# Performance work log

Hardware: AMD Instinct MI355X
Metric: run time of the kernel (lower is better)

The kernel has to match this reference:

```python
import jax, jax.numpy as jnp
import numpy as np

N_NODES = 50000
HIDDEN = 512
N_EDGES = 200000
NUM_LAYERS = 2


def setup_inputs() -> dict:
    key = jax.random.key(0)
    ks = jax.random.split(key, 8)
    stdv = 1.0 / np.sqrt(HIDDEN)
    u = lambda k, shape: jax.random.uniform(k, shape, jnp.float32, -stdv, stdv)
    inputs = jnp.arange(N_NODES, dtype=jnp.int64)
    A = jax.random.randint(ks[0], (2, N_EDGES), 0, N_NODES, dtype=jnp.int64)
    emb = u(ks[1], (N_NODES, HIDDEN))            # embedding table
    weight = u(ks[2], (NUM_LAYERS, HIDDEN, HIDDEN))  # per-layer edge transform
    w_ih = u(ks[3], (3 * HIDDEN, HIDDEN))        # GRUCell input weights (r,z,n)
    w_hh = u(ks[4], (3 * HIDDEN, HIDDEN))        # GRUCell hidden weights
    b_ih = u(ks[5], (3 * HIDDEN,))
    b_hh = u(ks[6], (3 * HIDDEN,))
    return {"inputs": inputs, "A": A, "emb": emb, "weight": weight,
            "w_ih": w_ih, "w_hh": w_hh, "b_ih": b_ih, "b_hh": b_hh}


def _gru_cell(m, h, w_ih, w_hh, b_ih, b_hh):
    # torch.nn.GRUCell math, gate order (r, z, n)
    gi = m @ w_ih.T + b_ih
    gh = h @ w_hh.T + b_hh
    i_r, i_z, i_n = jnp.split(gi, 3, axis=-1)
    h_r, h_z, h_n = jnp.split(gh, 3, axis=-1)
    r = jax.nn.sigmoid(i_r + h_r)
    z = jax.nn.sigmoid(i_z + h_z)
    n = jnp.tanh(i_n + r * h_n)
    return (1.0 - z) * n + z * h


def reference(inputs, A, emb, weight, w_ih, w_hh, b_ih, b_hh):
    x = emb[inputs]                      # [N, C] embedding gather
    src, dst = A[0], A[1]
    n = x.shape[0]
    for l in range(NUM_LAYERS):
        m = x @ weight[l]                # [N, C] per-layer transform
        agg = jax.ops.segment_sum(m[src], dst, num_segments=n)  # scatter-add messages
        x = _gru_cell(agg, x, w_ih, w_hh, b_ih, b_hh)
    return x
```

## Files before the change

### kernel.cpp

```cpp
#include <hip/hip_runtime.h>
#include <stdint.h>

#define N_NODES 50000
#define HIDDEN  512
#define N_EDGES 200000

#define BK 32
#define LDP 40
#define NBX ((N_NODES + 127) / 128)

typedef __attribute__((ext_vector_type(8)))  short short8;
typedef __attribute__((ext_vector_type(4)))  float floatx4;
typedef __attribute__((ext_vector_type(16))) float floatx16;

__device__ inline float bf2f(ushort u) {
    union { uint32_t u; float f; } v; v.u = ((uint32_t)u) << 16; return v.f;
}
__device__ inline ushort f2bf(float f) {
    union { float f; uint32_t u; } v; v.f = f;
    uint32_t r = v.u + 0x7fffu + ((v.u >> 16) & 1u);
    return (ushort)(r >> 16);
}
__device__ inline floatx4 mfma16(short8 a, short8 b, floatx4 c) {
    return __builtin_amdgcn_mfma_f32_16x16x32_bf16(a, b, c, 0, 0, 0);
}
__device__ inline floatx16 mfma32(short8 a, short8 b, floatx16 c) {
    return __builtin_amdgcn_mfma_f32_32x32x16_bf16(a, b, c, 0, 0, 0);
}
__device__ inline void gld16(const void* g, void* l) {
    __builtin_amdgcn_global_load_lds(
        (const __attribute__((address_space(1))) unsigned int*)g,
        (__attribute__((address_space(3))) unsigned int*)l, 16, 0, 0);
}
__device__ inline bool idx_is64(const int* __restrict__ inputs) {
    return inputs[1] == 0 && inputs[2] == 1;
}

__global__ void k_gather(const int* __restrict__ inputs, const float* __restrict__ emb,
                         ushort* __restrict__ xb) {
    bool is64 = idx_is64(inputs);
    int t = blockIdx.x * blockDim.x + threadIdx.x;
    int row = t >> 6, s8 = (t & 63) << 3;
    if (row >= N_NODES) return;
    int srow = is64 ? inputs[2 * row] : inputs[row];
    srow = srow < 0 ? 0 : (srow >= N_NODES ? N_NODES - 1 : srow);
    const float* src = emb + (size_t)srow * HIDDEN + s8;
    float4 v0 = *(const float4*)(src);
    float4 v1 = *(const float4*)(src + 4);
    ushort o[8] = { f2bf(v0.x), f2bf(v0.y), f2bf(v0.z), f2bf(v0.w),
                    f2bf(v1.x), f2bf(v1.y), f2bf(v1.z), f2bf(v1.w) };
    *(uint4*)(xb + (size_t)row * HIDDEN + s8) = *(uint4*)o;
}

__global__ void k_cvt8(const float* __restrict__ src, ushort* __restrict__ dst, int n) {
    int t = blockIdx.x * blockDim.x + threadIdx.x;
    int base = t * 8;
    if (base >= n) return;
    float4 v0 = *(const float4*)(src + base);
    float4 v1 = *(const float4*)(src + base + 4);
    ushort o[8] = { f2bf(v0.x), f2bf(v0.y), f2bf(v0.z), f2bf(v0.w),
                    f2bf(v1.x), f2bf(v1.y), f2bf(v1.z), f2bf(v1.w) };
    *(uint4*)(dst + base) = *(uint4*)o;
}

__device__ inline size_t wf_index(int grow, int k) {
    int g3 = grow >> 9, gcol = grow & 511;
    int cb = gcol >> 5, llo = gcol & 31;
    int kk = k >> 4, hi = (k >> 3) & 1, jj = k & 7;
    return ((((size_t)g3 * 16 + cb) * 32 + kk) * 64 + llo + hi * 32) * 8 + jj;
}

__global__ __launch_bounds__(256) void k_gemm_w(const ushort* __restrict__ Aw,
                                                const ushort* __restrict__ Bw,
                                                ushort* __restrict__ Cw) {
    __shared__ ushort As[128][LDP];
    __shared__ ushort Bs[128][LDP];
    const int l = blockIdx.z;
    const ushort* Bp = Bw + (size_t)l * HIDDEN * HIDDEN;
    ushort* Cp = Cw + (size_t)l * 3 * HIDDEN * HIDDEN;
    const int n0 = blockIdx.x * 128, c0 = blockIdx.y * 128;
    const int t = threadIdx.x;
    const int wave = t >> 6, lane = t & 63;
    const int wm = (wave >> 1) << 6, wn = (wave & 1) << 6;
    const int fr = lane & 15, fk = (lane >> 4) << 3;
    const int lm = t >> 2, lk = (t & 3) << 3;
    floatx4 acc[4][4] = {};

    for (int k0 = 0; k0 < HIDDEN; k0 += BK) {
        *(uint4*)&As[lm][lk]      = *(const uint4*)(Aw + (size_t)(n0 + lm) * HIDDEN + k0 + lk);
        *(uint4*)&As[64 + lm][lk] = *(const uint4*)(Aw + (size_t)(n0 + 64 + lm) * HIDDEN + k0 + lk);
        *(uint4*)&Bs[lm][lk]      = *(const uint4*)(Bp + (size_t)(c0 + lm) * HIDDEN + k0 + lk);
        *(uint4*)&Bs[64 + lm][lk] = *(const uint4*)(Bp + (size_t)(c0 + 64 + lm) * HIDDEN + k0 + lk);
        __syncthreads();
        short8 aa[4], bb[4];
        #pragma unroll
        for (int i = 0; i < 4; ++i) {
            aa[i] = *(const short8*)&As[wm + i * 16 + fr][fk];
            bb[i] = *(const short8*)&Bs[wn + i * 16 + fr][fk];
        }
        #pragma unroll
        for (int i = 0; i < 4; ++i)
            #pragma unroll
            for (int j = 0; j < 4; ++j)
                acc[i][j] = mfma16(aa[i], bb[j], acc[i][j]);
        __syncthreads();
    }
    const int er = (lane >> 4) << 2, ec = lane & 15;
    #pragma unroll
    for (int i = 0; i < 4; ++i)
        #pragma unroll
        for (int j = 0; j < 4; ++j)
            #pragma unroll
            for (int r = 0; r < 4; ++r) {
                int grow = n0 + wm + i * 16 + er + r;
                int kcol = c0 + wn + j * 16 + ec;
                Cp[wf_index(grow, kcol)] = f2bf(acc[i][j][r]);
            }
}

__global__ void k_pack_hh(const float* __restrict__ whh, ushort* __restrict__ wfh) {
    int t = blockIdx.x * blockDim.x + threadIdx.x;
    if (t >= 3 * HIDDEN * HIDDEN / 8) return;
    int grow = t >> 6, k = (t & 63) << 3;
    const float* src = whh + (size_t)grow * HIDDEN + k;
    ushort o[8];
    #pragma unroll
    for (int j = 0; j < 8; ++j) o[j] = f2bf(src[j]);
    *(uint4*)(wfh + wf_index(grow, k)) = *(uint4*)o;
}

__global__ void k_hist(const int* __restrict__ inputs, const int* __restrict__ A,
                       int* __restrict__ count) {
    bool is64 = idx_is64(inputs);
    int e = blockIdx.x * blockDim.x + threadIdx.x;
    if (e >= N_EDGES) return;
    int d = is64 ? A[2 * (N_EDGES + e)] : A[N_EDGES + e];
    if (d < 0 || d >= N_NODES) return;
    atomicAdd(count + d, 1);
}

#define SCAN_T 1024
__global__ __launch_bounds__(SCAN_T) void k_scan(const int* __restrict__ count,
                                                 int* __restrict__ row_start,
                                                 int* __restrict__ cursor) {
    __shared__ int part[SCAN_T];
    const int t = threadIdx.x;
    const int chunk = (N_NODES + SCAN_T - 1) / SCAN_T;
    const int base = t * chunk;
    int s = 0;
    for (int i = 0; i < chunk; ++i) {
        int idx = base + i;
        if (idx < N_NODES) s += count[idx];
    }
    part[t] = s;
    __syncthreads();
    for (int off = 1; off < SCAN_T; off <<= 1) {
        int add = (t >= off) ? part[t - off] : 0;
        __syncthreads();
        part[t] += add;
        __syncthreads();
    }
    int running = (t == 0) ? 0 : part[t - 1];
    for (int i = 0; i < chunk; ++i) {
        int idx = base + i;
        if (idx < N_NODES) {
            row_start[idx] = running;
            cursor[idx] = running;
            running += count[idx];
        }
    }
    if (t == 0) row_start[N_NODES] = part[SCAN_T - 1];
}

__global__ void k_place(const int* __restrict__ inputs, const int* __restrict__ A,
                        int* __restrict__ cursor, int* __restrict__ esrc) {
    bool is64 = idx_is64(inputs);
    int e = blockIdx.x * blockDim.x + threadIdx.x;
    if (e >= N_EDGES) return;
    int s, d;
    if (is64) { s = A[2 * e]; d = A[2 * (N_EDGES + e)]; }
    else      { s = A[e];     d = A[N_EDGES + e]; }
    if (s < 0 || s >= N_NODES || d < 0 || d >= N_NODES) return;
    int pos = atomicAdd(cursor + d, 1);
    esrc[pos] = s;
}

__global__ __launch_bounds__(256) void k_agg(const int* __restrict__ row_start,
                                             const int* __restrict__ esrc,
                                             const ushort* __restrict__ x,
                                             ushort* __restrict__ ax) {
    int node = blockIdx.x * 4 + (threadIdx.x >> 6);
    if (node >= N_NODES) return;
    int lane = threadIdx.x & 63;
    int q = lane << 3;
    int beg = row_start[node], end = row_start[node + 1];
    float acc[8] = {};
    for (int i = beg; i < end; ++i) {
        int s = esrc[i];
        uint4 v = *(const uint4*)(x + (size_t)s * HIDDEN + q);
        const ushort* u = (const ushort*)&v;
        #pragma unroll
        for (int j = 0; j < 8; ++j) acc[j] += bf2f(u[j]);
    }
    ushort o[8];
    #pragma unroll
    for (int j = 0; j < 8; ++j) o[j] = f2bf(acc[j]);
    *(uint4*)(ax + (size_t)node * HIDDEN + q) = *(uint4*)o;
}

template<bool F32OUT>
__global__ __launch_bounds__(256, 2) void k_gru5(
    const ushort* __restrict__ agg, const ushort* __restrict__ xb_cur,
    const ushort* __restrict__ wfc,
    const ushort* __restrict__ wfh,
    const float* __restrict__ b_ih, const float* __restrict__ b_hh,
    ushort* __restrict__ outB, float* __restrict__ outF)
{
    __shared__ ushort S[2 * 20480];
    const int x  = blockIdx.x & 7;
    const int n  = blockIdx.x >> 3;
    const int by = n & 7;
    const int bx = x + ((n >> 3) << 3);
    if (bx >= NBX) return;
    const int n0 = bx * 128;
    const int t = threadIdx.x, w = t >> 6, lane = t & 63;
    const int lrow = lane & 31, lhi = lane >> 5;
    const int wr = w >> 1, wc = w & 1;
    const int wrow = wr << 6;
    const int cb = by * 2 + wc;

    floatx16 a_sr[2] = {}, a_sz[2] = {}, a_in[2] = {}, a_hn[2] = {};

    const ushort* wB[6] = { wfc, wfc + 262144, wfc + 524288,
                            wfh, wfh + 262144, wfh + 524288 };

    const ushort* sp[10];
    int           adv[10];
    int           off[10];
    #pragma unroll
    for (int q = 0; q < 10; ++q) {
        const int F = w * 10 + q;
        const int kk = F / 20, s = F % 20;
        off[q] = kk * 10240 + s * 512;
        if (s < 8) {
            const int rg = s & 3;
            int row = n0 + rg * 32 + lrow;
            if (row >= N_NODES) row = N_NODES - 1;
            const ushort* arr = (s < 4) ? agg : xb_cur;
            sp[q] = arr + (size_t)row * HIDDEN + kk * 16 + lhi * 8;
            adv[q] = 32;
        } else {
            const int g = (s - 8) >> 1, c = (s - 8) & 1;
            const int cbq = by * 2 + c;
            sp[q] = wB[g] + ((size_t)(cbq * 32 + kk) * 64 + lane) * 8;
            adv[q] = 1024;
        }
    }

    #pragma unroll
    for (int q = 0; q < 10; ++q) { gld16(sp[q], S + off[q]); sp[q] += adv[q]; }
    __syncthreads();

    for (int ks = 0; ks < 16; ++ks) {
        const int cur = ks & 1;
        if (ks + 1 < 16) {
            ushort* dst = S + (cur ^ 1) * 20480;
            #pragma unroll
            for (int q = 0; q < 10; ++q) { gld16(sp[q], dst + off[q]); sp[q] += adv[q]; }
        }
        const ushort* Bb = S + cur * 20480 + (size_t)lane * 8;
        #pragma unroll
        for (int kk = 0; kk < 2; ++kk) {
            const ushort* P = Bb + kk * 10240;
            short8 av0 = *(const short8*)(P + (wr * 2 + 0) * 512);
            short8 av1 = *(const short8*)(P + (wr * 2 + 1) * 512);
            short8 xv0 = *(const short8*)(P + (4 + wr * 2 + 0) * 512);
            short8 xv1 = *(const short8*)(P + (4 + wr * 2 + 1) * 512);
            short8 B0 = *(const short8*)(P + (8 +  0 + wc) * 512);
            short8 B1 = *(const short8*)(P + (8 +  2 + wc) * 512);
            short8 B2 = *(const short8*)(P + (8 +  4 + wc) * 512);
            short8 B3 = *(const short8*)(P + (8 +  6 + wc) * 512);
            short8 B4 = *(const short8*)(P + (8 +  8 + wc) * 512);
            short8 B5 = *(const short8*)(P + (8 + 10 + wc) * 512);
            a_sr[0] = mfma32(av0, B0, a_sr[0]);  a_sr[0] = mfma32(xv0, B3, a_sr[0]);
            a_sr[1] = mfma32(av1, B0, a_sr[1]);  a_sr[1] = mfma32(xv1, B3, a_sr[1]);
            a_sz[0] = mfma32(av0, B1, a_sz[0]);  a_sz[0] = mfma32(xv0, B4, a_sz[0]);
            a_sz[1] = mfma32(av1, B1, a_sz[1]);  a_sz[1] = mfma32(xv1, B4, a_sz[1]);
            a_in[0] = mfma32(av0, B2, a_in[0]);  a_in[1] = mfma32(av1, B2, a_in[1]);
            a_hn[0] = mfma32(xv0, B5, a_hn[0]);  a_hn[1] = mfma32(xv1, B5, a_hn[1]);
        }
        __syncthreads();
    }
    const int colL = (cb << 5) + lrow;
    const float bir = b_ih[colL] + b_hh[colL];
    const float biz = b_ih[HIDDEN + colL] + b_hh[HIDDEN + colL];
    const float bin = b_ih[2 * HIDDEN + colL];
    const float bhn = b_hh[2 * HIDDEN + colL];
    #pragma unroll
    for (int rf = 0; rf < 2; ++rf) {
        #pragma unroll
        for (int rg = 0; rg < 16; ++rg) {
            const int row = n0 + wrow + rf * 32 + (rg & 3) + ((rg >> 2) << 3) + (lhi << 2);
            if (row >= N_NODES) continue;
            float vsr = a_sr[rf][rg] + bir;
            float vsz = a_sz[rf][rg] + biz;
            float vin = a_in[rf][rg] + bin;
            float vhn = a_hn[rf][rg] + bhn;
            float rr = 1.f / (1.f + __expf(-vsr));
            float zz = 1.f / (1.f + __expf(-vsz));
            float nn = tanhf(vin + rr * vhn);
            float h  = bf2f(xb_cur[(size_t)row * HIDDEN + colL]);
            float out = (1.f - zz) * nn + zz * h;
            if (F32OUT) outF[(size_t)row * HIDDEN + colL] = out;
            else        outB[(size_t)row * HIDDEN + colL] = f2bf(out);
        }
    }
}

extern "C" void kernel_launch(void* const* d_in, const int* in_sizes, int n_in,
                              void* d_out, int out_size, void* d_ws, size_t ws_size,
                              hipStream_t stream) {
    const int*   inputs = (const int*)d_in[0];
    const int*   A      = (const int*)d_in[1];
    const float* emb    = (const float*)d_in[2];
    const float* weight = (const float*)d_in[3];
    const float* w_ih   = (const float*)d_in[4];
    const float* w_hh   = (const float*)d_in[5];
    const float* b_ih   = (const float*)d_in[6];
    const float* b_hh   = (const float*)d_in[7];

    char* ws = (char*)d_ws;
    size_t off = 0;
    auto alloc = [&](size_t bytes) { void* p = ws + off; off += (bytes + 255) & ~255ull; return p; };
    ushort* WihB      = (ushort*)alloc((size_t)3 * HIDDEN * HIDDEN * sizeof(ushort));
    ushort* Wb        = (ushort*)alloc((size_t)2 * HIDDEN * HIDDEN * sizeof(ushort));
    ushort* WFc       = (ushort*)alloc((size_t)2 * 3 * HIDDEN * HIDDEN * sizeof(ushort));
    ushort* WFhh      = (ushort*)alloc((size_t)3 * HIDDEN * HIDDEN * sizeof(ushort));
    ushort* bufA      = (ushort*)alloc((size_t)N_NODES * HIDDEN * sizeof(ushort));
    ushort* bufB      = (ushort*)alloc((size_t)N_NODES * HIDDEN * sizeof(ushort));
    int*    count     = (int*)alloc((size_t)N_NODES * sizeof(int));
    int*    row_start = (int*)alloc((size_t)(N_NODES + 1) * sizeof(int));
    int*    cursor    = (int*)alloc((size_t)N_NODES * sizeof(int));
    int*    esrc      = (int*)alloc((size_t)N_EDGES * sizeof(int));
    ushort* ax0       = (ushort*)d_out;

    const int nW3 = 3 * HIDDEN * HIDDEN, nW2 = 2 * HIDDEN * HIDDEN;
    const size_t WF_L = (size_t)3 * HIDDEN * HIDDEN;

    k_cvt8<<<(nW3 / 8 + 255) / 256, 256, 0, stream>>>(w_ih, WihB, nW3);
    k_cvt8<<<(nW2 / 8 + 255) / 256, 256, 0, stream>>>(weight, Wb, nW2);
    k_pack_hh<<<(nW3 / 8 + 255) / 256, 256, 0, stream>>>(w_hh, WFhh);
    k_gemm_w<<<dim3(12, 4, 2), 256, 0, stream>>>(WihB, Wb, WFc);

    k_gather<<<(N_NODES * 64 + 255) / 256, 256, 0, stream>>>(inputs, emb, bufA);

    hipMemsetAsync(count, 0, (size_t)N_NODES * sizeof(int), stream);
    k_hist<<<(N_EDGES + 255) / 256, 256, 0, stream>>>(inputs, A, count);
    k_scan<<<1, SCAN_T, 0, stream>>>(count, row_start, cursor);
    k_place<<<(N_EDGES + 255) / 256, 256, 0, stream>>>(inputs, A, cursor, esrc);

    dim3 gGru(8 * 8 * ((NBX + 7) / 8));
    dim3 ga((N_NODES + 3) / 4);

    k_agg<<<ga, 256, 0, stream>>>(row_start, esrc, bufA, ax0);
    k_gru5<false><<<gGru, 256, 0, stream>>>(ax0, bufA, WFc, WFhh, b_ih, b_hh, bufB, nullptr);

    k_agg<<<ga, 256, 0, stream>>>(row_start, esrc, bufB, bufA);
    k_gru5<true><<<gGru, 256, 0, stream>>>(bufA, bufB, WFc + WF_L, WFhh, b_ih, b_hh,
                                           nullptr, (float*)d_out);
}
```

Baseline: 932.5 us.

## Load GRU GEMM operands directly from global memory instead of LDS staging

The fused GRU GEMM kernel stops staging activation and weight fragments through a double-buffered LDS tile with global_load_lds and barriers. Each wave now loads its MFMA operands straight from global memory into registers in a 32-step unrolled loop. This removes the LDS traffic and block-wide synchronisation. In exchange, tiles shared between waves are no longer reused through LDS, which increases global and L2 load traffic and leaves latency hiding to the unrolled loads.

```diff
diff --git a/kernel.cpp b/kernel.cpp
--- a/kernel.cpp
+++ b/kernel.cpp
@@ -26,11 +26,6 @@
 }
 __device__ inline floatx16 mfma32(short8 a, short8 b, floatx16 c) {
     return __builtin_amdgcn_mfma_f32_32x32x16_bf16(a, b, c, 0, 0, 0);
-}
-__device__ inline void gld16(const void* g, void* l) {
-    __builtin_amdgcn_global_load_lds(
-        (const __attribute__((address_space(1))) unsigned int*)g,
-        (__attribute__((address_space(3))) unsigned int*)l, 16, 0, 0);
 }
 __device__ inline bool idx_is64(const int* __restrict__ inputs) {
     return inputs[1] == 0 && inputs[2] == 1;
@@ -209,14 +204,13 @@
 }
 
 template<bool F32OUT>
-__global__ __launch_bounds__(256, 2) void k_gru5(
+__global__ __launch_bounds__(256, 2) void k_gru7(
     const ushort* __restrict__ agg, const ushort* __restrict__ xb_cur,
     const ushort* __restrict__ wfc,
     const ushort* __restrict__ wfh,
     const float* __restrict__ b_ih, const float* __restrict__ b_hh,
     ushort* __restrict__ outB, float* __restrict__ outF)
 {
-    __shared__ ushort S[2 * 20480];
     const int x  = blockIdx.x & 7;
     const int n  = blockIdx.x >> 3;
     const int by = n & 7;
@@ -231,66 +225,40 @@
 
     floatx16 a_sr[2] = {}, a_sz[2] = {}, a_in[2] = {}, a_hn[2] = {};
 
-    const ushort* wB[6] = { wfc, wfc + 262144, wfc + 524288,
-                            wfh, wfh + 262144, wfh + 524288 };
-
-    const ushort* sp[10];
-    int           adv[10];
-    int           off[10];
-    #pragma unroll
-    for (int q = 0; q < 10; ++q) {
-        const int F = w * 10 + q;
-        const int kk = F / 20, s = F % 20;
-        off[q] = kk * 10240 + s * 512;
-        if (s < 8) {
-            const int rg = s & 3;
-            int row = n0 + rg * 32 + lrow;
-            if (row >= N_NODES) row = N_NODES - 1;
-            const ushort* arr = (s < 4) ? agg : xb_cur;
-            sp[q] = arr + (size_t)row * HIDDEN + kk * 16 + lhi * 8;
-            adv[q] = 32;
-        } else {
-            const int g = (s - 8) >> 1, c = (s - 8) & 1;
-            const int cbq = by * 2 + c;
-            sp[q] = wB[g] + ((size_t)(cbq * 32 + kk) * 64 + lane) * 8;
-            adv[q] = 1024;
-        }
-    }
-
-    #pragma unroll
-    for (int q = 0; q < 10; ++q) { gld16(sp[q], S + off[q]); sp[q] += adv[q]; }
-    __syncthreads();
-
-    for (int ks = 0; ks < 16; ++ks) {
-        const int cur = ks & 1;
-        if (ks + 1 < 16) {
-            ushort* dst = S + (cur ^ 1) * 20480;
-            #pragma unroll
-            for (int q = 0; q < 10; ++q) { gld16(sp[q], dst + off[q]); sp[q] += adv[q]; }
-        }
-        const ushort* Bb = S + cur * 20480 + (size_t)lane * 8;
-        #pragma unroll
-        for (int kk = 0; kk < 2; ++kk) {
-            const ushort* P = Bb + kk * 10240;
-            short8 av0 = *(const short8*)(P + (wr * 2 + 0) * 512);
-            short8 av1 = *(const short8*)(P + (wr * 2 + 1) * 512);
-            short8 xv0 = *(const short8*)(P + (4 + wr * 2 + 0) * 512);
-            short8 xv1 = *(const short8*)(P + (4 + wr * 2 + 1) * 512);
-            short8 B0 = *(const short8*)(P + (8 +  0 + wc) * 512);
-            short8 B1 = *(const short8*)(P + (8 +  2 + wc) * 512);
-            short8 B2 = *(const short8*)(P + (8 +  4 + wc) * 512);
-            short8 B3 = *(const short8*)(P + (8 +  6 + wc) * 512);
-            short8 B4 = *(const short8*)(P + (8 +  8 + wc) * 512);
-            short8 B5 = *(const short8*)(P + (8 + 10 + wc) * 512);
-            a_sr[0] = mfma32(av0, B0, a_sr[0]);  a_sr[0] = mfma32(xv0, B3, a_sr[0]);
-            a_sr[1] = mfma32(av1, B0, a_sr[1]);  a_sr[1] = mfma32(xv1, B3, a_sr[1]);
-            a_sz[0] = mfma32(av0, B1, a_sz[0]);  a_sz[0] = mfma32(xv0, B4, a_sz[0]);
-            a_sz[1] = mfma32(av1, B1, a_sz[1]);  a_sz[1] = mfma32(xv1, B4, a_sz[1]);
-            a_in[0] = mfma32(av0, B2, a_in[0]);  a_in[1] = mfma32(av1, B2, a_in[1]);
-            a_hn[0] = mfma32(xv0, B5, a_hn[0]);  a_hn[1] = mfma32(xv1, B5, a_hn[1]);
-        }
-        __syncthreads();
-    }
+    int r0 = n0 + wrow + lrow;       if (r0 >= N_NODES) r0 = N_NODES - 1;
+    int r1 = n0 + wrow + 32 + lrow;  if (r1 >= N_NODES) r1 = N_NODES - 1;
+    const ushort* pa0 = agg    + (size_t)r0 * HIDDEN + lhi * 8;
+    const ushort* pa1 = agg    + (size_t)r1 * HIDDEN + lhi * 8;
+    const ushort* px0 = xb_cur + (size_t)r0 * HIDDEN + lhi * 8;
+    const ushort* px1 = xb_cur + (size_t)r1 * HIDDEN + lhi * 8;
+    const size_t wo = ((size_t)cb * 32) * 512 + (size_t)lane * 8;
+    const ushort* pw0 = wfc            + wo;
+    const ushort* pw1 = wfc + 262144   + wo;
+    const ushort* pw2 = wfc + 524288   + wo;
+    const ushort* pw3 = wfh            + wo;
+    const ushort* pw4 = wfh + 262144   + wo;
+    const ushort* pw5 = wfh + 524288   + wo;
+
+    #pragma unroll 4
+    for (int kk = 0; kk < 32; ++kk) {
+        short8 av0 = *(const short8*)(pa0 + kk * 16);
+        short8 av1 = *(const short8*)(pa1 + kk * 16);
+        short8 xv0 = *(const short8*)(px0 + kk * 16);
+        short8 xv1 = *(const short8*)(px1 + kk * 16);
+        short8 B0  = *(const short8*)(pw0 + (size_t)kk * 512);
+        short8 B1  = *(const short8*)(pw1 + (size_t)kk * 512);
+        short8 B2  = *(const short8*)(pw2 + (size_t)kk * 512);
+        short8 B3  = *(const short8*)(pw3 + (size_t)kk * 512);
+        short8 B4  = *(const short8*)(pw4 + (size_t)kk * 512);
+        short8 B5  = *(const short8*)(pw5 + (size_t)kk * 512);
+        a_sr[0] = mfma32(av0, B0, a_sr[0]);  a_sr[0] = mfma32(xv0, B3, a_sr[0]);
+        a_sr[1] = mfma32(av1, B0, a_sr[1]);  a_sr[1] = mfma32(xv1, B3, a_sr[1]);
+        a_sz[0] = mfma32(av0, B1, a_sz[0]);  a_sz[0] = mfma32(xv0, B4, a_sz[0]);
+        a_sz[1] = mfma32(av1, B1, a_sz[1]);  a_sz[1] = mfma32(xv1, B4, a_sz[1]);
+        a_in[0] = mfma32(av0, B2, a_in[0]);  a_in[1] = mfma32(av1, B2, a_in[1]);
+        a_hn[0] = mfma32(xv0, B5, a_hn[0]);  a_hn[1] = mfma32(xv1, B5, a_hn[1]);
+    }
+
     const int colL = (cb << 5) + lrow;
     const float bir = b_ih[colL] + b_hh[colL];
     const float biz = b_ih[HIDDEN + colL] + b_hh[HIDDEN + colL];
@@ -363,9 +331,9 @@
     dim3 ga((N_NODES + 3) / 4);
 
     k_agg<<<ga, 256, 0, stream>>>(row_start, esrc, bufA, ax0);
-    k_gru5<false><<<gGru, 256, 0, stream>>>(ax0, bufA, WFc, WFhh, b_ih, b_hh, bufB, nullptr);
+    k_gru7<false><<<gGru, 256, 0, stream>>>(ax0, bufA, WFc, WFhh, b_ih, b_hh, bufB, nullptr);
 
     k_agg<<<ga, 256, 0, stream>>>(row_start, esrc, bufB, bufA);
-    k_gru5<true><<<gGru, 256, 0, stream>>>(bufA, bufB, WFc + WF_L, WFhh, b_ih, b_hh,
+    k_gru7<true><<<gGru, 256, 0, stream>>>(bufA, bufB, WFc + WF_L, WFhh, b_ih, b_hh,
                                            nullptr, (float*)d_out);
 }
```

Result: slower. 1.178 ms (+26.3%).

## Widen GRU tile to eight waves with per-phase pipelined LDS loads

Applied to the files above, without the earlier changes.

The fused GRU GEMM kernel moves from 4 waves covering 128x64 output columns to 8 waves covering 128x128 columns, halving the grid. The K-loop is split into four phases. Each phase waits with a partial vmcnt and a raw barrier, then issues the next stage's global-to-LDS loads and its MFMAs under raised priority. The aim is to improve operand reuse per block and overlap memory traffic with matrix math at finer granularity. The cost is a larger LDS footprint, which likely limits occupancy, and prefetches on the last iteration that read past the useful K range.

```diff
diff --git a/kernel.cpp b/kernel.cpp
--- a/kernel.cpp
+++ b/kernel.cpp
@@ -209,88 +209,82 @@
 }
 
 template<bool F32OUT>
-__global__ __launch_bounds__(256, 2) void k_gru5(
+__global__ __launch_bounds__(512, 2) void k_gru8(
     const ushort* __restrict__ agg, const ushort* __restrict__ xb_cur,
     const ushort* __restrict__ wfc,
     const ushort* __restrict__ wfh,
     const float* __restrict__ b_ih, const float* __restrict__ b_hh,
     ushort* __restrict__ outB, float* __restrict__ outF)
 {
-    __shared__ ushort S[2 * 20480];
+    __shared__ ushort S[2 * 32768];
     const int x  = blockIdx.x & 7;
     const int n  = blockIdx.x >> 3;
-    const int by = n & 7;
-    const int bx = x + ((n >> 3) << 3);
+    const int by = n & 3;
+    const int bx = x + ((n >> 2) << 3);
     if (bx >= NBX) return;
     const int n0 = bx * 128;
     const int t = threadIdx.x, w = t >> 6, lane = t & 63;
     const int lrow = lane & 31, lhi = lane >> 5;
-    const int wr = w >> 1, wc = w & 1;
-    const int wrow = wr << 6;
-    const int cb = by * 2 + wc;
+    const int wr = w >> 2, wc = w & 3;
+    const int cb0 = by * 4;
+    const int cb = cb0 + wc;
 
     floatx16 a_sr[2] = {}, a_sz[2] = {}, a_in[2] = {}, a_hn[2] = {};
 
     const ushort* wB[6] = { wfc, wfc + 262144, wfc + 524288,
                             wfh, wfh + 262144, wfh + 524288 };
 
-    const ushort* sp[10];
-    int           adv[10];
-    int           off[10];
-    #pragma unroll
-    for (int q = 0; q < 10; ++q) {
-        const int F = w * 10 + q;
-        const int kk = F / 20, s = F % 20;
-        off[q] = kk * 10240 + s * 512;
-        if (s < 8) {
-            const int rg = s & 3;
-            int row = n0 + rg * 32 + lrow;
+    const ushort* sp[8];
+    int           adv[8];
+    int           off[8];
+    #pragma unroll
+    for (int q = 0; q < 8; ++q) {
+        const int p = q >> 1, e = q & 1;
+        const int f = 2 * w + e;
+        const int sub = p & 1, kh = p >> 1;
+        off[q] = (p * 16 + f) * 512;
+        if (f < 4) {
+            int row = n0 + f * 32 + lrow;
             if (row >= N_NODES) row = N_NODES - 1;
-            const ushort* arr = (s < 4) ? agg : xb_cur;
-            sp[q] = arr + (size_t)row * HIDDEN + kk * 16 + lhi * 8;
+            const ushort* arr = sub ? xb_cur : agg;
+            sp[q] = arr + (size_t)row * HIDDEN + kh * 16 + lhi * 8;
             adv[q] = 32;
         } else {
-            const int g = (s - 8) >> 1, c = (s - 8) & 1;
-            const int cbq = by * 2 + c;
-            sp[q] = wB[g] + ((size_t)(cbq * 32 + kk) * 64 + lane) * 8;
+            const int fw = f - 4, j = fw >> 2, cbl = fw & 3, g = j + 3 * sub;
+            sp[q] = wB[g] + ((size_t)(cb0 + cbl) * 32 + kh) * 512 + (size_t)lane * 8;
             adv[q] = 1024;
         }
     }
 
     #pragma unroll
-    for (int q = 0; q < 10; ++q) { gld16(sp[q], S + off[q]); sp[q] += adv[q]; }
-    __syncthreads();
+    for (int q = 0; q < 8; ++q) { gld16(sp[q], S + off[q]); sp[q] += adv[q]; }
+
+    #define PHASE(p, A0, A1, A2)  {                                                  \
+        asm volatile("s_waitcnt vmcnt(6)\n\ts_barrier" ::: "memory");                \
+        const ushort* P = S + (size_t)cur * 32768 + (p) * 16 * 512 + (size_t)lane * 8;\
+        short8 v0 = *(const short8*)(P + (wr * 2 + 0) * 512);                        \
+        short8 v1 = *(const short8*)(P + (wr * 2 + 1) * 512);                        \
+        short8 W0 = *(const short8*)(P + (4 + 0 * 4 + wc) * 512);                    \
+        short8 W1 = *(const short8*)(P + (4 + 1 * 4 + wc) * 512);                    \
+        short8 W2 = *(const short8*)(P + (4 + 2 * 4 + wc) * 512);                    \
+        ushort* D = S + (size_t)(cur ^ 1) * 32768;                                   \
+        gld16(sp[(p) * 2 + 0], D + off[(p) * 2 + 0]); sp[(p) * 2 + 0] += adv[(p) * 2 + 0]; \
+        gld16(sp[(p) * 2 + 1], D + off[(p) * 2 + 1]); sp[(p) * 2 + 1] += adv[(p) * 2 + 1]; \
+        __builtin_amdgcn_s_setprio(1);                                               \
+        A0[0] = mfma32(v0, W0, A0[0]);  A0[1] = mfma32(v1, W0, A0[1]);               \
+        A1[0] = mfma32(v0, W1, A1[0]);  A1[1] = mfma32(v1, W1, A1[1]);               \
+        A2[0] = mfma32(v0, W2, A2[0]);  A2[1] = mfma32(v1, W2, A2[1]);               \
+        __builtin_amdgcn_s_setprio(0); }
 
     for (int ks = 0; ks < 16; ++ks) {
         const int cur = ks & 1;
-        if (ks + 1 < 16) {
-            ushort* dst = S + (cur ^ 1) * 20480;
-            #pragma unroll
-            for (int q = 0; q < 10; ++q) { gld16(sp[q], dst + off[q]); sp[q] += adv[q]; }
-        }
-        const ushort* Bb = S + cur * 20480 + (size_t)lane * 8;
-        #pragma unroll
-        for (int kk = 0; kk < 2; ++kk) {
-            const ushort* P = Bb + kk * 10240;
-            short8 av0 = *(const short8*)(P + (wr * 2 + 0) * 512);
-            short8 av1 = *(const short8*)(P + (wr * 2 + 1) * 512);
-            short8 xv0 = *(const short8*)(P + (4 + wr * 2 + 0) * 512);
-            short8 xv1 = *(const short8*)(P + (4 + wr * 2 + 1) * 512);
-            short8 B0 = *(const short8*)(P + (8 +  0 + wc) * 512);
-            short8 B1 = *(const short8*)(P + (8 +  2 + wc) * 512);
-            short8 B2 = *(const short8*)(P + (8 +  4 + wc) * 512);
-            short8 B3 = *(const short8*)(P + (8 +  6 + wc) * 512);
-            short8 B4 = *(const short8*)(P + (8 +  8 + wc) * 512);
-            short8 B5 = *(const short8*)(P + (8 + 10 + wc) * 512);
-            a_sr[0] = mfma32(av0, B0, a_sr[0]);  a_sr[0] = mfma32(xv0, B3, a_sr[0]);
-            a_sr[1] = mfma32(av1, B0, a_sr[1]);  a_sr[1] = mfma32(xv1, B3, a_sr[1]);
-            a_sz[0] = mfma32(av0, B1, a_sz[0]);  a_sz[0] = mfma32(xv0, B4, a_sz[0]);
-            a_sz[1] = mfma32(av1, B1, a_sz[1]);  a_sz[1] = mfma32(xv1, B4, a_sz[1]);
-            a_in[0] = mfma32(av0, B2, a_in[0]);  a_in[1] = mfma32(av1, B2, a_in[1]);
-            a_hn[0] = mfma32(xv0, B5, a_hn[0]);  a_hn[1] = mfma32(xv1, B5, a_hn[1]);
-        }
-        __syncthreads();
-    }
+        PHASE(0, a_sr, a_sz, a_in)
+        PHASE(1, a_sr, a_sz, a_hn)
+        PHASE(2, a_sr, a_sz, a_in)
+        PHASE(3, a_sr, a_sz, a_hn)
+    }
+    #undef PHASE
+
     const int colL = (cb << 5) + lrow;
     const float bir = b_ih[colL] + b_hh[colL];
     const float biz = b_ih[HIDDEN + colL] + b_hh[HIDDEN + colL];
@@ -300,7 +294,7 @@
     for (int rf = 0; rf < 2; ++rf) {
         #pragma unroll
         for (int rg = 0; rg < 16; ++rg) {
-            const int row = n0 + wrow + rf * 32 + (rg & 3) + ((rg >> 2) << 3) + (lhi << 2);
+            const int row = n0 + wr * 64 + rf * 32 + (rg & 3) + ((rg >> 2) << 3) + (lhi << 2);
             if (row >= N_NODES) continue;
             float vsr = a_sr[rf][rg] + bir;
             float vsz = a_sz[rf][rg] + biz;
@@ -359,13 +353,13 @@
     k_scan<<<1, SCAN_T, 0, stream>>>(count, row_start, cursor);
     k_place<<<(N_EDGES + 255) / 256, 256, 0, stream>>>(inputs, A, cursor, esrc);
 
-    dim3 gGru(8 * 8 * ((NBX + 7) / 8));
+    dim3 gGru(8 * 4 * ((NBX + 7) / 8));
     dim3 ga((N_NODES + 3) / 4);
 
     k_agg<<<ga, 256, 0, stream>>>(row_start, esrc, bufA, ax0);
-    k_gru5<false><<<gGru, 256, 0, stream>>>(ax0, bufA, WFc, WFhh, b_ih, b_hh, bufB, nullptr);
+    k_gru8<false><<<gGru, 512, 0, stream>>>(ax0, bufA, WFc, WFhh, b_ih, b_hh, bufB, nullptr);
 
     k_agg<<<ga, 256, 0, stream>>>(row_start, esrc, bufB, bufA);
-    k_gru5<true><<<gGru, 256, 0, stream>>>(bufA, bufB, WFc + WF_L, WFhh, b_ih, b_hh,
+    k_gru8<true><<<gGru, 512, 0, stream>>>(bufA, bufB, WFc + WF_L, WFhh, b_ih, b_hh,
                                            nullptr, (float*)d_out);
 }
```

After: 900.7 us. 3.4% less time.
